# Optimization experiments

Measured on AMD Instinct MI355X. Metric: run time of the kernel, lower is better.

The kernel has to match this reference:

```python
import jax, jax.numpy as jnp
import numpy as np

INPUT_DIM = 1024
HIDDEN_DIM = 2048
NUM_EMB = 4096
EMB_DIM = 256
N = 65536


def setup_inputs() -> dict:
    key = jax.random.key(0)
    ks = jax.random.split(key, 10)
    s = lambda fan_in: 1.0 / np.sqrt(fan_in)
    return {
        "x": jax.random.normal(ks[0], (N, INPUT_DIM), dtype=jnp.float32),
        # encoder: Linear(input_dim, hidden) -> ReLU -> Linear(hidden, emb)
        "W1": jax.random.uniform(ks[1], (INPUT_DIM, HIDDEN_DIM), jnp.float32, -s(INPUT_DIM), s(INPUT_DIM)),
        "b1": jax.random.uniform(ks[2], (HIDDEN_DIM,), jnp.float32, -s(INPUT_DIM), s(INPUT_DIM)),
        "W2": jax.random.uniform(ks[3], (HIDDEN_DIM, EMB_DIM), jnp.float32, -s(HIDDEN_DIM), s(HIDDEN_DIM)),
        "b2": jax.random.uniform(ks[4], (EMB_DIM,), jnp.float32, -s(HIDDEN_DIM), s(HIDDEN_DIM)),
        # codebook (nn.Embedding weight)
        "codebook": jax.random.normal(ks[5], (NUM_EMB, EMB_DIM), dtype=jnp.float32),
        # decoder: Linear(emb, hidden) -> ReLU -> Linear(hidden, input_dim)
        "W3": jax.random.uniform(ks[6], (EMB_DIM, HIDDEN_DIM), jnp.float32, -s(EMB_DIM), s(EMB_DIM)),
        "b3": jax.random.uniform(ks[7], (HIDDEN_DIM,), jnp.float32, -s(EMB_DIM), s(EMB_DIM)),
        "W4": jax.random.uniform(ks[8], (HIDDEN_DIM, INPUT_DIM), jnp.float32, -s(HIDDEN_DIM), s(HIDDEN_DIM)),
        "b4": jax.random.uniform(ks[9], (INPUT_DIM,), jnp.float32, -s(HIDDEN_DIM), s(HIDDEN_DIM)),
    }


def reference(x, W1, b1, W2, b2, codebook, W3, b3, W4, b4):
    # encoder
    h = jax.nn.relu(x @ W1 + b1)
    encoded = h @ W2 + b2                      # [N, E]
    # cdist (squared form; argmin is identical to Euclidean argmin)
    enc_sq = jnp.sum(encoded * encoded, axis=-1, keepdims=True)   # [N, 1]
    cb_sq = jnp.sum(codebook * codebook, axis=-1)                 # [K]
    d2 = enc_sq - 2.0 * (encoded @ codebook.T) + cb_sq            # [N, K]
    indices = jnp.argmin(d2, axis=-1)                             # [N]
    quantized = codebook[indices]                                 # [N, E]
    # decoder
    h2 = jax.nn.relu(quantized @ W3 + b3)
    decoded = h2 @ W4 + b4
    return (quantized, decoded)
```

## Files before the change

### kernel.cpp

```cpp
#include <hip/hip_runtime.h>

#define N_ROWS 65536
#define IN_DIM 1024
#define HID    2048
#define EMB    256
#define NCODE  4096

typedef __attribute__((ext_vector_type(8))) short bf16x8;
typedef __attribute__((ext_vector_type(4))) float f32x4;

__device__ __forceinline__ unsigned short f2bf(float v) {
    unsigned u = __float_as_uint(v);
    u += 0x7FFFu + ((u >> 16) & 1u);
    return (unsigned short)(u >> 16);
}
__device__ __forceinline__ float bf2f(unsigned short h) {
    return __uint_as_float(((unsigned)h) << 16);
}
__device__ __forceinline__ void gload16(const unsigned short* g, unsigned short* l) {
    __builtin_amdgcn_global_load_lds(
        (const __attribute__((address_space(1))) unsigned int*)g,
        (__attribute__((address_space(3))) unsigned int*)l, 16, 0, 0);
}

template<int SPLIT>
__global__ __launch_bounds__(256) void k_conv_w(
    const float* __restrict__ src, unsigned short* __restrict__ dh,
    unsigned short* __restrict__ dl, int NC, int nkt)
{
    const int t = threadIdx.x;
    const int nt = blockIdx.x, kt = blockIdx.y;
    const int kk = t >> 2, j4 = (t & 3) << 2;
    const int k0 = kt << 6, n0 = nt << 4;
    float4 v = *(const float4*)(src + (size_t)(k0 + kk) * NC + n0 + j4);
    size_t tb = ((size_t)nt * nkt + kt) * 1024 + ((kk >> 3) * 128) + (kk & 7);
    float vv[4] = {v.x, v.y, v.z, v.w};
    #pragma unroll
    for (int j = 0; j < 4; ++j) {
        unsigned short h = f2bf(vv[j]);
        dh[tb + (size_t)(j4 + j) * 8] = h;
        if (SPLIT) dl[tb + (size_t)(j4 + j) * 8] = f2bf(vv[j] - bf2f(h));
    }
}

__global__ __launch_bounds__(256) void k_conv_a2(
    const float* __restrict__ src, unsigned short* __restrict__ dh,
    unsigned short* __restrict__ dl, int Kw, int nkt)
{
    const int t = threadIdx.x;
    const int mt = blockIdx.x, kt = blockIdx.y;
    const int rr = t >> 4, k4 = (t & 15) << 2;
    float4 v = *(const float4*)(src + (size_t)(mt * 16 + rr) * Kw + kt * 64 + k4);
    size_t addr = ((size_t)mt * nkt + kt) * 1024 + (k4 >> 3) * 128 + rr * 8 + (k4 & 7);
    ushort4 h = { f2bf(v.x), f2bf(v.y), f2bf(v.z), f2bf(v.w) };
    ushort4 lo = { f2bf(v.x - bf2f(h.x)), f2bf(v.y - bf2f(h.y)),
                   f2bf(v.z - bf2f(h.z)), f2bf(v.w - bf2f(h.w)) };
    *(ushort4*)&dh[addr] = h;
    *(ushort4*)&dl[addr] = lo;
}

__global__ __launch_bounds__(256) void k_conv_cb(
    const float* __restrict__ cb, unsigned short* __restrict__ ch,
    unsigned short* __restrict__ cl_, float* __restrict__ halfsq)
{
    const int t = threadIdx.x;
    const int ct = blockIdx.x;
    const int cl = t >> 4, f = t & 15;
    const int code = (ct << 4) + cl;
    float ssq = 0.f;
    #pragma unroll
    for (int it = 0; it < 4; ++it) {
        const int k4 = (f << 2) + (it << 6);
        float4 v = *(const float4*)(cb + (size_t)code * EMB + k4);
        ssq += v.x * v.x + v.y * v.y + v.z * v.z + v.w * v.w;
        size_t tb = ((size_t)(ct * 4 + (k4 >> 6))) * 1024 + ((k4 >> 3) & 7) * 128 + cl * 8 + (k4 & 7);
        ushort4 h = { f2bf(v.x), f2bf(v.y), f2bf(v.z), f2bf(v.w) };
        *(ushort4*)&ch[tb] = h;
        ushort4 lo = { f2bf(v.x - bf2f(h.x)), f2bf(v.y - bf2f(h.y)),
                       f2bf(v.z - bf2f(h.z)), f2bf(v.w - bf2f(h.w)) };
        *(ushort4*)&cl_[tb] = lo;
    }
    #pragma unroll
    for (int off = 1; off <= 8; off <<= 1) ssq += __shfl_xor(ssq, off);
    if (f == 0) halfsq[code] = 0.5f * ssq;
}

__global__ __launch_bounds__(512, 2) void k_gemm1(
    const unsigned short* __restrict__ At, const unsigned short* __restrict__ Atl,
    int a_nkt,
    const unsigned short* __restrict__ Bh, const unsigned short* __restrict__ Bl,
    int b_nkt, int K,
    const float* __restrict__ bias,
    unsigned short* __restrict__ outt, unsigned short* __restrict__ outt2,
    int out_nkt)
{
    constexpr int BUFSZ = 16384;
    __shared__ __align__(16) unsigned short s_mem[2 * BUFSZ];

    const int t = threadIdx.x;
    const int id = blockIdx.x;
    const int m_low = id & 7, rest = id >> 3;
    const int nb = rest & 15;
    const int m0 = (((rest >> 4) << 3) | m_low) * 128;
    const int nb0 = nb * 128;
    const int lane = t & 63, wv = t >> 6;
    const int wm = wv >> 2, wn = wv & 3;
    const int g = lane >> 4, rr = lane & 15;
    const int nt = K >> 6;

    f32x4 acc[4][2];
    #pragma unroll
    for (int mi = 0; mi < 4; ++mi)
        #pragma unroll
        for (int ni = 0; ni < 2; ++ni) acc[mi][ni] = (f32x4){0.f, 0.f, 0.f, 0.f};

    #define G1_STAGE(buf, ktile)                                                       \
        {                                                                              \
            unsigned short* base_ = &s_mem[(buf) * BUFSZ];                             \
            const size_t ga_ = ((size_t)(m0 / 16 + wv) * a_nkt + (ktile)) * 1024;      \
            const size_t gb_ = ((size_t)((nb0 >> 4) + wv) * b_nkt + (ktile)) * 1024;   \
            _Pragma("unroll")                                                          \
            for (int hf = 0; hf < 2; ++hf) {                                           \
                gload16(At + ga_ + hf * 512 + lane * 8, base_ + wv * 1024 + hf * 512); \
                gload16(Bh + gb_ + hf * 512 + lane * 8, base_ + 8192 + wv * 1024 + hf * 512); \
            }                                                                          \
        }

    #define G1_COMPUTE(buf, ktile)                                                     \
        {                                                                              \
            const unsigned short* base_ = &s_mem[(buf) * BUFSZ];                       \
            __builtin_amdgcn_s_setprio(1);                                             \
            _Pragma("unroll")                                                          \
            for (int s = 0; s < 2; ++s) {                                              \
                const int kb = (s << 2) + g;                                           \
                bf16x8 a_h[4], a_l[4], b_h[2], b_l[2];                                 \
                _Pragma("unroll")                                                      \
                for (int i = 0; i < 4; ++i) {                                          \
                    int aaddr = (wm * 4 + i) * 1024 + kb * 128 + (rr << 3);            \
                    a_h[i] = *(const bf16x8*)&base_[aaddr];                            \
                    a_l[i] = *(const bf16x8*)(Atl +                                    \
                        ((size_t)(m0 / 16 + wm * 4 + i) * a_nkt + (ktile)) * 1024      \
                        + kb * 128 + (rr << 3));                                       \
                }                                                                      \
                _Pragma("unroll")                                                      \
                for (int j = 0; j < 2; ++j) {                                          \
                    int baddr = 8192 + (wn * 2 + j) * 1024 + kb * 128 + (rr << 3);     \
                    b_h[j] = *(const bf16x8*)&base_[baddr];                            \
                    b_l[j] = *(const bf16x8*)(Bl +                                     \
                        ((size_t)((nb0 >> 4) + wn * 2 + j) * b_nkt + (ktile)) * 1024   \
                        + kb * 128 + (rr << 3));                                       \
                }                                                                      \
                _Pragma("unroll")                                                      \
                for (int mi = 0; mi < 4; ++mi)                                         \
                    _Pragma("unroll")                                                  \
                    for (int ni = 0; ni < 2; ++ni) {                                   \
                        acc[mi][ni] = __builtin_amdgcn_mfma_f32_16x16x32_bf16(a_h[mi], b_h[ni], acc[mi][ni], 0, 0, 0); \
                        acc[mi][ni] = __builtin_amdgcn_mfma_f32_16x16x32_bf16(a_l[mi], b_h[ni], acc[mi][ni], 0, 0, 0); \
                        acc[mi][ni] = __builtin_amdgcn_mfma_f32_16x16x32_bf16(a_h[mi], b_l[ni], acc[mi][ni], 0, 0, 0); \
                    }                                                                  \
            }                                                                          \
            __builtin_amdgcn_s_setprio(0);                                             \
        }

    G1_STAGE(0, 0)
    asm volatile("s_waitcnt vmcnt(0)" ::: "memory");
    __builtin_amdgcn_s_barrier();
    __builtin_amdgcn_sched_barrier(0);

    int cur = 0;
    for (int kt = 0; kt < nt; ++kt) {
        if (kt + 1 < nt) G1_STAGE(cur ^ 1, kt + 1)
        G1_COMPUTE(cur, kt)
        asm volatile("s_waitcnt vmcnt(0)" ::: "memory");
        __builtin_amdgcn_s_barrier();
        __builtin_amdgcn_sched_barrier(0);
        cur ^= 1;
    }
    #undef G1_STAGE
    #undef G1_COMPUTE

    for (int pass = 0; pass < 2; ++pass) {
        #pragma unroll
        for (int mi = 0; mi < 4; ++mi)
            #pragma unroll
            for (int ni = 0; ni < 2; ++ni) {
                const int c = wn * 32 + ni * 16 + rr;
                float bb = bias[nb0 + c];
                const int ktl = c >> 6, k = c & 63;
                #pragma unroll
                for (int rg = 0; rg < 4; ++rg) {
                    float v = fmaxf(acc[mi][ni][rg] + bb, 0.f);
                    unsigned short hi = f2bf(v);
                    unsigned short w = (pass == 0) ? hi : f2bf(v - bf2f(hi));
                    int addr = ((wm * 4 + mi) * 2 + ktl) * 1024
                             + ((k >> 3) & 7) * 128 + (g * 4 + rg) * 8 + (k & 7);
                    s_mem[addr] = w;
                }
            }
        __syncthreads();
        unsigned short* dst = (pass == 0) ? outt : outt2;
        #pragma unroll
        for (int it = 0; it < 4; ++it) {
            int f = t + (it << 9);
            int tl = f >> 7, w8 = f & 127;
            size_t gaddr = ((size_t)(m0 / 16 + (tl >> 1)) * out_nkt + (nb0 >> 6) + (tl & 1)) * 1024;
            *(float4*)(dst + gaddr + w8 * 8) = *(const float4*)&s_mem[tl * 1024 + w8 * 8];
        }
        __syncthreads();
    }
}

__global__ __launch_bounds__(512, 1) void k_gemm2(
    const unsigned short* __restrict__ At, const unsigned short* __restrict__ Atl,
    int a_nkt,
    const unsigned short* __restrict__ Bh, const unsigned short* __restrict__ Bl,
    int b_nkt, int K,
    const float* __restrict__ bias, float* __restrict__ out)
{
    constexpr int BUFSZ = 24576;
    __shared__ __align__(16) unsigned short s_mem[2 * BUFSZ];

    const int t = threadIdx.x;
    const int m0 = blockIdx.x * 64;
    const int lane = t & 63, wv = t >> 6;
    const int wm = wv >> 2, wn = wv & 3;
    const int g = lane >> 4, rr = lane & 15;
    const int nt = K >> 6;

    f32x4 acc[2][4];
    #pragma unroll
    for (int mi = 0; mi < 2; ++mi)
        #pragma unroll
        for (int ni = 0; ni < 4; ++ni) acc[mi][ni] = (f32x4){0.f, 0.f, 0.f, 0.f};

    #define G2_STAGE(buf, ktile)                                                       \
        {                                                                              \
            unsigned short* base_ = &s_mem[(buf) * BUFSZ];                             \
            _Pragma("unroll")                                                          \
            for (int jj = 0; jj < 2; ++jj) {                                           \
                const int j_ = wv * 2 + jj;                                            \
                const size_t gb_ = ((size_t)j_ * b_nkt + (ktile)) * 1024;              \
                _Pragma("unroll")                                                      \
                for (int hf = 0; hf < 2; ++hf)                                         \
                    gload16(Bh + gb_ + hf * 512 + lane * 8,                            \
                            base_ + 8192 + j_ * 1024 + hf * 512);                      \
            }                                                                          \
            const int at_ = wv & 3;                                                    \
            const size_t ga_ = ((size_t)(m0 / 16 + at_) * a_nkt + (ktile)) * 1024;     \
            if (wv < 4) {                                                              \
                _Pragma("unroll")                                                      \
                for (int hf = 0; hf < 2; ++hf)                                         \
                    gload16(At + ga_ + hf * 512 + lane * 8,                            \
                            base_ + at_ * 1024 + hf * 512);                            \
            } else {                                                                   \
                _Pragma("unroll")                                                      \
                for (int hf = 0; hf < 2; ++hf)                                         \
                    gload16(Atl + ga_ + hf * 512 + lane * 8,                           \
                            base_ + 4096 + at_ * 1024 + hf * 512);                     \
            }                                                                          \
        }

    #define G2_COMPUTE(buf, ktile)                                                     \
        {                                                                              \
            const unsigned short* base_ = &s_mem[(buf) * BUFSZ];                       \
            __builtin_amdgcn_s_setprio(1);                                             \
            _Pragma("unroll")                                                          \
            for (int s = 0; s < 2; ++s) {                                              \
                const int kb = (s << 2) + g;                                           \
                bf16x8 a_h[2], a_l[2], b_h[4], b_l[4];                                 \
                _Pragma("unroll")                                                      \
                for (int i = 0; i < 2; ++i) {                                          \
                    int aaddr = (wm * 2 + i) * 1024 + kb * 128 + (rr << 3);            \
                    a_h[i] = *(const bf16x8*)&base_[aaddr];                            \
                    a_l[i] = *(const bf16x8*)&base_[4096 + aaddr];                     \
                }                                                                      \
                _Pragma("unroll")                                                      \
                for (int j = 0; j < 4; ++j) {                                          \
                    int baddr = 8192 + (wn * 4 + j) * 1024 + kb * 128 + (rr << 3);     \
                    b_h[j] = *(const bf16x8*)&base_[baddr];                            \
                    b_l[j] = *(const bf16x8*)(Bl +                                     \
                        ((size_t)(wn * 4 + j) * b_nkt + (ktile)) * 1024                \
                        + kb * 128 + (rr << 3));                                       \
                }                                                                      \
                _Pragma("unroll")                                                      \
                for (int mi = 0; mi < 2; ++mi)                                         \
                    _Pragma("unroll")                                                  \
                    for (int ni = 0; ni < 4; ++ni) {                                   \
                        acc[mi][ni] = __builtin_amdgcn_mfma_f32_16x16x32_bf16(a_h[mi], b_h[ni], acc[mi][ni], 0, 0, 0); \
                        acc[mi][ni] = __builtin_amdgcn_mfma_f32_16x16x32_bf16(a_l[mi], b_h[ni], acc[mi][ni], 0, 0, 0); \
                        acc[mi][ni] = __builtin_amdgcn_mfma_f32_16x16x32_bf16(a_h[mi], b_l[ni], acc[mi][ni], 0, 0, 0); \
                    }                                                                  \
            }                                                                          \
            __builtin_amdgcn_s_setprio(0);                                             \
        }

    G2_STAGE(0, 0)
    asm volatile("s_waitcnt vmcnt(0)" ::: "memory");
    __builtin_amdgcn_s_barrier();
    __builtin_amdgcn_sched_barrier(0);

    int cur = 0;
    for (int kt = 0; kt < nt; ++kt) {
        if (kt + 1 < nt) G2_STAGE(cur ^ 1, kt + 1)
        G2_COMPUTE(cur, kt)
        asm volatile("s_waitcnt vmcnt(0)" ::: "memory");
        __builtin_amdgcn_s_barrier();
        __builtin_amdgcn_sched_barrier(0);
        cur ^= 1;
    }
    #undef G2_STAGE
    #undef G2_COMPUTE

    float* sf = (float*)s_mem;
    #pragma unroll
    for (int mi = 0; mi < 2; ++mi)
        #pragma unroll
        for (int ni = 0; ni < 4; ++ni)
            #pragma unroll
            for (int rg = 0; rg < 4; ++rg)
                sf[(wm * 32 + mi * 16 + g * 4 + rg) * 256 + wn * 64 + ni * 16 + rr] = acc[mi][ni][rg];
    __syncthreads();
    #pragma unroll
    for (int it = 0; it < 8; ++it) {
        int f = t + (it << 9);
        int r = f >> 6, c4 = (f & 63) << 2;
        float4 v = *(const float4*)&sf[r * 256 + c4];
        v.x += bias[c4 + 0]; v.y += bias[c4 + 1];
        v.z += bias[c4 + 2]; v.w += bias[c4 + 3];
        *(float4*)(out + (size_t)(m0 + r) * EMB + c4) = v;
    }
}

template<int SPLIT, int AFMT, int OUTT>
__global__ __launch_bounds__(512, 1) void k_layer2(
    const float* __restrict__ A, const unsigned short* __restrict__ At,
    const unsigned short* __restrict__ Atl, int a_nkt,
    int lda, int K,
    const unsigned short* __restrict__ Bh, const unsigned short* __restrict__ Bl,
    int b_nkt, const float* __restrict__ bias, int biasoff,
    float* __restrict__ out, unsigned short* __restrict__ outt,
    unsigned short* __restrict__ outt2,
    int outw, int relu, int init, int ny_log2)
{
    constexpr int BUFSZ = SPLIT ? 32768 : 24576;
    constexpr int AL = 8192;
    constexpr int BH = SPLIT ? 16384 : 8192;
    __shared__ __align__(16) unsigned short s_mem[2 * BUFSZ];

    const int t = threadIdx.x;
    const int id = blockIdx.x;
    const int m_low = id & 7, rest = id >> 3;
    const int nb = rest & ((1 << ny_log2) - 1);
    const int m0 = (((rest >> ny_log2) << 3) | m_low) * 128;
    const int nb0 = nb * 256;
    const int lane = t & 63, wv = t >> 6;
    const int wm = wv >> 2, wn = wv & 3;
    const int g = lane >> 4, rr = lane & 15;
    const int nt = K >> 6;

    f32x4 acc[4][4];
    #pragma unroll
    for (int mi = 0; mi < 4; ++mi)
        #pragma unroll
        for (int ni = 0; ni < 4; ++ni) acc[mi][ni] = (f32x4){0.f, 0.f, 0.f, 0.f};

    #define STAGE_DMA(buf, ktile)                                                      \
        {                                                                              \
            unsigned short* base_ = &s_mem[(buf) * BUFSZ];                             \
            _Pragma("unroll")                                                          \
            for (int jj = 0; jj < 2; ++jj) {                                           \
                const int j_ = wv * 2 + jj;                                            \
                const size_t gt_ = ((size_t)(nb0 / 16 + j_) * b_nkt + (ktile)) * 1024; \
                _Pragma("unroll")                                                      \
                for (int hf = 0; hf < 2; ++hf)                                         \
                    gload16(Bh + gt_ + hf * 512 + lane * 8,                            \
                            base_ + BH + j_ * 1024 + hf * 512);                        \
            }                                                                          \
            if (AFMT >= 1) {                                                           \
                const size_t ga_ = ((size_t)(m0 / 16 + wv) * a_nkt + (ktile)) * 1024;  \
                _Pragma("unroll")                                                      \
                for (int hf = 0; hf < 2; ++hf)                                         \
                    gload16(At + ga_ + hf * 512 + lane * 8,                            \
                            base_ + wv * 1024 + hf * 512);                             \
                if (AFMT == 2) {                                                       \
                    _Pragma("unroll")                                                  \
                    for (int hf = 0; hf < 2; ++hf)                                     \
                        gload16(Atl + ga_ + hf * 512 + lane * 8,                       \
                                base_ + AL + wv * 1024 + hf * 512);                    \
                }                                                                      \
            }                                                                          \
        }

    #define A_LOAD(ktile, pv)                                                          \
        {                                                                              \
            _Pragma("unroll")                                                          \
            for (int it = 0; it < 4; ++it) {                                           \
                int f_ = t + (it << 9);                                                \
                int r_ = f_ >> 4, k4_ = (f_ & 15) << 2;                                \
                pv[it] = *(const float4*)(A + (size_t)(m0 + r_) * lda + (ktile) * 64 + k4_); \
            }                                                                          \
        }

    #define A_WRITE(buf, pv)                                                           \
        {                                                                              \
            unsigned short* base_ = &s_mem[(buf) * BUFSZ];                             \
            _Pragma("unroll")                                                          \
            for (int it = 0; it < 4; ++it) {                                           \
                int f_ = t + (it << 9);                                                \
                int r_ = f_ >> 4, k4_ = (f_ & 15) << 2;                                \
                int mt_ = r_ >> 4, rl_ = r_ & 15, kb_ = k4_ >> 3, e_ = k4_ & 7;        \
                int addr_ = mt_ * 1024 + kb_ * 128 + ((rl_ ^ kb_) << 3) + e_;          \
                float4 v_ = pv[it];                                                    \
                ushort4 hi_, lo_;                                                      \
                hi_.x = f2bf(v_.x); hi_.y = f2bf(v_.y); hi_.z = f2bf(v_.z); hi_.w = f2bf(v_.w); \
                *(ushort4*)&base_[addr_] = hi_;                                        \
                if (SPLIT) {                                                           \
                    lo_.x = f2bf(v_.x - bf2f(hi_.x)); lo_.y = f2bf(v_.y - bf2f(hi_.y)); \
                    lo_.z = f2bf(v_.z - bf2f(hi_.z)); lo_.w = f2bf(v_.w - bf2f(hi_.w)); \
                    *(ushort4*)&base_[AL + addr_] = lo_;                               \
                }                                                                      \
            }                                                                          \
        }

    #define COMPUTE(buf, ktile)                                                        \
        {                                                                              \
            const unsigned short* base_ = &s_mem[(buf) * BUFSZ];                       \
            __builtin_amdgcn_s_setprio(1);                                             \
            _Pragma("unroll")                                                          \
            for (int s = 0; s < 2; ++s) {                                              \
                const int kb = (s << 2) + g;                                           \
                bf16x8 a_h[4], a_l[4], b_h[4], b_l[4];                                 \
                _Pragma("unroll")                                                      \
                for (int i = 0; i < 4; ++i) {                                          \
                    int arow = (AFMT == 0) ? (((rr ^ kb) & 15) << 3) : (rr << 3);      \
                    int aaddr = (wm * 4 + i) * 1024 + kb * 128 + arow;                 \
                    a_h[i] = *(const bf16x8*)&base_[aaddr];                            \
                    if (SPLIT) a_l[i] = *(const bf16x8*)&base_[AL + aaddr];            \
                    int baddr = (wn * 4 + i) * 1024 + kb * 128 + (rr << 3);            \
                    b_h[i] = *(const bf16x8*)&base_[BH + baddr];                       \
                    if (SPLIT)                                                         \
                        b_l[i] = *(const bf16x8*)(Bl +                                 \
                            ((size_t)(nb0 / 16 + wn * 4 + i) * b_nkt + (ktile)) * 1024 \
                            + kb * 128 + (rr << 3));                                   \
                }                                                                      \
                _Pragma("unroll")                                                      \
                for (int mi = 0; mi < 4; ++mi)                                         \
                    _Pragma("unroll")                                                  \
                    for (int ni = 0; ni < 4; ++ni) {                                   \
                        acc[mi][ni] = __builtin_amdgcn_mfma_f32_16x16x32_bf16(a_h[mi], b_h[ni], acc[mi][ni], 0, 0, 0); \
                        if (SPLIT) {                                                   \
                            acc[mi][ni] = __builtin_amdgcn_mfma_f32_16x16x32_bf16(a_l[mi], b_h[ni], acc[mi][ni], 0, 0, 0); \
                            acc[mi][ni] = __builtin_amdgcn_mfma_f32_16x16x32_bf16(a_h[mi], b_l[ni], acc[mi][ni], 0, 0, 0); \
                        }                                                              \
                    }                                                                  \
            }                                                                          \
            __builtin_amdgcn_s_setprio(0);                                             \
        }

    float4 pv[4];
    STAGE_DMA(0, 0)
    if (AFMT == 0) {
        A_LOAD(0, pv)
        A_WRITE(0, pv)
    }
    asm volatile("s_waitcnt vmcnt(0) lgkmcnt(0)" ::: "memory");
    __builtin_amdgcn_s_barrier();
    __builtin_amdgcn_sched_barrier(0);

    int cur = 0;
    for (int kt = 0; kt < nt; ++kt) {
        if (kt + 1 < nt) {
            STAGE_DMA(cur ^ 1, kt + 1)
            if (AFMT == 0) A_LOAD(kt + 1, pv)
        }
        COMPUTE(cur, kt)
        if (AFMT == 0) { if (kt + 1 < nt) A_WRITE(cur ^ 1, pv) }
        asm volatile("s_waitcnt vmcnt(0) lgkmcnt(0)" ::: "memory");
        __builtin_amdgcn_s_barrier();
        __builtin_amdgcn_sched_barrier(0);
        cur ^= 1;
    }
    #undef STAGE_DMA
    #undef A_LOAD
    #undef A_WRITE
    #undef COMPUTE

    if (OUTT == 0) {
        float* sf = (float*)s_mem;
        for (int rm = 0; rm < 2; ++rm) {
            if (wm == rm) {
                #pragma unroll
                for (int mi = 0; mi < 4; ++mi)
                    #pragma unroll
                    for (int ni = 0; ni < 4; ++ni)
                        #pragma unroll
                        for (int rg = 0; rg < 4; ++rg)
                            sf[(mi * 16 + g * 4 + rg) * 256 + wn * 64 + ni * 16 + rr] = acc[mi][ni][rg];
            }
            __syncthreads();
            #pragma unroll
            for (int it = 0; it < 8; ++it) {
                int f = t + (it << 9);
                int r = f >> 6, c4 = (f & 63) << 2;
                float4 v = *(const float4*)&sf[r * 256 + c4];
                int gr = m0 + rm * 64 + r, gc = nb0 + c4;
                float* op = out + (size_t)gr * outw + gc;
                if (init) {
                    v.x += bias[biasoff + gc + 0]; v.y += bias[biasoff + gc + 1];
                    v.z += bias[biasoff + gc + 2]; v.w += bias[biasoff + gc + 3];
                } else {
                    float4 o = *(const float4*)op;
                    v.x += o.x; v.y += o.y; v.z += o.z; v.w += o.w;
                }
                if (relu) {
                    v.x = fmaxf(v.x, 0.f); v.y = fmaxf(v.y, 0.f);
                    v.z = fmaxf(v.z, 0.f); v.w = fmaxf(v.w, 0.f);
                }
                *(float4*)op = v;
            }
            __syncthreads();
        }
    } else {
        const int npass = (OUTT == 2) ? 2 : 1;
        for (int pass = 0; pass < npass; ++pass) {
            #pragma unroll
            for (int mi = 0; mi < 4; ++mi)
                #pragma unroll
                for (int ni = 0; ni < 4; ++ni) {
                    const int c = wn * 64 + ni * 16 + rr;
                    float bb = bias[biasoff + nb0 + c];
                    #pragma unroll
                    for (int rg = 0; rg < 4; ++rg) {
                        float v = acc[mi][ni][rg] + bb;
                        if (relu) v = fmaxf(v, 0.f);
                        unsigned short hi = f2bf(v);
                        unsigned short w = (pass == 0) ? hi : f2bf(v - bf2f(hi));
                        int addr = ((wm * 4 + mi) * 4 + wn) * 1024
                                 + (ni * 2 + (rr >> 3)) * 128 + (g * 4 + rg) * 8 + (rr & 7);
                        s_mem[addr] = w;
                    }
                }
            __syncthreads();
            unsigned short* dst = (pass == 0) ? outt : outt2;
            #pragma unroll
            for (int it = 0; it < 8; ++it) {
                int f = t + (it << 9);
                int tl = f >> 7, w8 = f & 127;
                size_t gaddr = ((size_t)(m0 / 16 + (tl >> 2)) * outw + nb0 / 64 + (tl & 3)) * 1024;
                *(float4*)(dst + gaddr + w8 * 8) = *(const float4*)&s_mem[tl * 1024 + w8 * 8];
            }
            __syncthreads();
        }
    }
}

__global__ __launch_bounds__(512, 1) void k_dist(
    float* encq, const unsigned short* __restrict__ ch,
    const unsigned short* __restrict__ cl,
    const float* __restrict__ hsq, const float* __restrict__ cb,
    unsigned short* __restrict__ qt)
{
    __shared__ __align__(16) unsigned short s_cb[3][16384];
    __shared__ int s_c1[256], s_c2[256];

    const int t = threadIdx.x;
    const int lane = t & 63, wv = t >> 6;
    const int g = lane >> 4, rr = lane & 15;
    const int r0 = blockIdx.x * 256;

    bf16x8 eh[2][8], el[2][8];
    #pragma unroll
    for (int rg = 0; rg < 2; ++rg) {
        const float* ep = encq + (size_t)(r0 + wv * 32 + rg * 16 + rr) * EMB + g * 8;
        #pragma unroll
        for (int s = 0; s < 8; ++s) {
            float4 v0 = *(const float4*)(ep + s * 32);
            float4 v1 = *(const float4*)(ep + s * 32 + 4);
            float vv[8] = {v0.x, v0.y, v0.z, v0.w, v1.x, v1.y, v1.z, v1.w};
            bf16x8 a, b;
            #pragma unroll
            for (int j = 0; j < 8; ++j) {
                unsigned short h = f2bf(vv[j]);
                a[j] = (short)h;
                b[j] = (short)f2bf(vv[j] - bf2f(h));
            }
            eh[rg][s] = a; el[rg][s] = b;
        }
    }
    float b1v[2][4], b2v[2][4]; int i1v[2][4], i2v[2][4];
    #pragma unroll
    for (int rg = 0; rg < 2; ++rg)
        #pragma unroll
        for (int r2 = 0; r2 < 4; ++r2) {
            b1v[rg][r2] = -1e30f; b2v[rg][r2] = -1e30f;
            i1v[rg][r2] = 0; i2v[rg][r2] = 0;
        }

    #define STAGE(buf, c)                                                              \
        {                                                                              \
            const unsigned short* gh_ = ch + (size_t)(c) * 8192 + wv * 1024;           \
            const unsigned short* gl_ = cl + (size_t)(c) * 8192 + wv * 1024;           \
            _Pragma("unroll")                                                          \
            for (int i_ = 0; i_ < 2; ++i_) {                                           \
                gload16(gh_ + i_ * 512 + lane * 8, &s_cb[buf][wv * 1024 + i_ * 512]);  \
                gload16(gl_ + i_ * 512 + lane * 8, &s_cb[buf][8192 + wv * 1024 + i_ * 512]); \
            }                                                                          \
        }

    #define COMPUTE(cur, c, hv_)                                                       \
        {                                                                              \
            f32x4 ahh[2][2], ahl[2][2], alh[2][2];                                     \
            _Pragma("unroll")                                                          \
            for (int rg = 0; rg < 2; ++rg)                                             \
                _Pragma("unroll")                                                      \
                for (int ci = 0; ci < 2; ++ci) {                                       \
                    ahh[rg][ci] = (f32x4){0.f, 0.f, 0.f, 0.f};                         \
                    ahl[rg][ci] = (f32x4){0.f, 0.f, 0.f, 0.f};                         \
                    alh[rg][ci] = (f32x4){0.f, 0.f, 0.f, 0.f};                         \
                }                                                                      \
            __builtin_amdgcn_s_setprio(1);                                             \
            _Pragma("unroll")                                                          \
            for (int s = 0; s < 8; ++s) {                                              \
                const int ktile = s >> 1, kb = ((s & 1) << 2) + g;                     \
                _Pragma("unroll")                                                      \
                for (int ci = 0; ci < 2; ++ci) {                                       \
                    const int off = (ci * 4 + ktile) * 1024 + kb * 128 + rr * 8;       \
                    bf16x8 bh = *(const bf16x8*)&s_cb[cur][off];                       \
                    bf16x8 bl = *(const bf16x8*)&s_cb[cur][8192 + off];                \
                    _Pragma("unroll")                                                  \
                    for (int rg = 0; rg < 2; ++rg) {                                   \
                        ahh[rg][ci] = __builtin_amdgcn_mfma_f32_16x16x32_bf16(eh[rg][s], bh, ahh[rg][ci], 0, 0, 0); \
                        ahl[rg][ci] = __builtin_amdgcn_mfma_f32_16x16x32_bf16(eh[rg][s], bl, ahl[rg][ci], 0, 0, 0); \
                        alh[rg][ci] = __builtin_amdgcn_mfma_f32_16x16x32_bf16(el[rg][s], bh, alh[rg][ci], 0, 0, 0); \
                    }                                                                  \
                }                                                                      \
            }                                                                          \
            __builtin_amdgcn_s_setprio(0);                                             \
            _Pragma("unroll")                                                          \
            for (int rg = 0; rg < 2; ++rg)                                             \
                _Pragma("unroll")                                                      \
                for (int ci = 0; ci < 2; ++ci) {                                       \
                    f32x4 av = ahh[rg][ci] + ahl[rg][ci] + alh[rg][ci];                \
                    const int code = ((c) << 5) + (ci << 4) + rr;                      \
                    const float hs = __shfl(hv_, ci * 16 + rr);                        \
                    _Pragma("unroll")                                                  \
                    for (int r2 = 0; r2 < 4; ++r2) {                                   \
                        float v = av[r2] - hs;                                         \
                        bool bt1 = (v > b1v[rg][r2]) || (v == b1v[rg][r2] && code < i1v[rg][r2]); \
                        bool bt2 = (v > b2v[rg][r2]) || (v == b2v[rg][r2] && code < i2v[rg][r2]); \
                        if (bt1) { b2v[rg][r2] = b1v[rg][r2]; i2v[rg][r2] = i1v[rg][r2]; \
                                   b1v[rg][r2] = v; i1v[rg][r2] = code; }              \
                        else if (bt2) { b2v[rg][r2] = v; i2v[rg][r2] = code; }         \
                    }                                                                  \
                }                                                                      \
        }

    STAGE(0, 0)
    int bufc = 0;
    for (int c = 0; c < 128; ++c) {
        const int bufn = (bufc == 2) ? 0 : bufc + 1;
        if (c + 1 < 128) STAGE(bufn, c + 1)
        float hv_ = hsq[(c << 5) + (lane & 31)];
        if (c + 1 < 128) asm volatile("s_waitcnt vmcnt(5)" ::: "memory");
        else             asm volatile("s_waitcnt vmcnt(0)" ::: "memory");
        __builtin_amdgcn_s_barrier();
        __builtin_amdgcn_sched_barrier(0);
        COMPUTE(bufc, c, hv_)
        bufc = bufn;
    }
    #undef STAGE
    #undef COMPUTE

    #pragma unroll
    for (int off = 1; off <= 8; off <<= 1) {
        #pragma unroll
        for (int rg = 0; rg < 2; ++rg)
            #pragma unroll
            for (int r2 = 0; r2 < 4; ++r2) {
                float ob1 = __shfl_xor(b1v[rg][r2], off), ob2 = __shfl_xor(b2v[rg][r2], off);
                int oi1 = __shfl_xor(i1v[rg][r2], off), oi2 = __shfl_xor(i2v[rg][r2], off);
                bool ofirst = (ob1 > b1v[rg][r2]) || (ob1 == b1v[rg][r2] && oi1 < i1v[rg][r2]);
                if (ofirst) {
                    bool mysec = (b1v[rg][r2] > ob2) || (b1v[rg][r2] == ob2 && i1v[rg][r2] < oi2);
                    b2v[rg][r2] = mysec ? b1v[rg][r2] : ob2; i2v[rg][r2] = mysec ? i1v[rg][r2] : oi2;
                    b1v[rg][r2] = ob1; i1v[rg][r2] = oi1;
                } else {
                    bool osec = (ob1 > b2v[rg][r2]) || (ob1 == b2v[rg][r2] && oi1 < i2v[rg][r2]);
                    b2v[rg][r2] = osec ? ob1 : b2v[rg][r2]; i2v[rg][r2] = osec ? oi1 : i2v[rg][r2];
                }
            }
    }
    if (rr == 0) {
        #pragma unroll
        for (int rg = 0; rg < 2; ++rg)
            #pragma unroll
            for (int r2 = 0; r2 < 4; ++r2) {
                int rl = wv * 32 + rg * 16 + g * 4 + r2;
                s_c1[rl] = i1v[rg][r2]; s_c2[rl] = i2v[rg][r2];
            }
    }
    __syncthreads();

    for (int rloc = 0; rloc < 32; ++rloc) {
        const int row = wv * 32 + rloc;
        const int c1 = s_c1[row], c2 = s_c2[row];
        float4 ev = *(const float4*)(encq + (size_t)(r0 + row) * EMB + lane * 4);
        float4 v1 = *(const float4*)(cb + (size_t)c1 * EMB + lane * 4);
        float4 v2 = *(const float4*)(cb + (size_t)c2 * EMB + lane * 4);
        float d1 = ev.x * v1.x + ev.y * v1.y + ev.z * v1.z + ev.w * v1.w;
        float d2 = ev.x * v2.x + ev.y * v2.y + ev.z * v2.z + ev.w * v2.w;
        #pragma unroll
        for (int off = 1; off <= 32; off <<= 1) {
            d1 += __shfl_xor(d1, off);
            d2 += __shfl_xor(d2, off);
        }
        if (lane == 0) {
            float s1 = d1 - hsq[c1], s2 = d2 - hsq[c2];
            bool keep1 = (s1 > s2) || (s1 == s2 && c1 < c2);
            s_c1[row] = keep1 ? c1 : c2;
        }
    }
    __syncthreads();
    #pragma unroll
    for (int it = 0; it < 32; ++it) {
        int f = t + (it << 9);
        int row = f >> 6, c4 = (f & 63) << 2;
        int bi = s_c1[row];
        float4 qv = *(const float4*)(cb + (size_t)bi * EMB + c4);
        const int R = r0 + row;
        *(float4*)(encq + (size_t)R * EMB + c4) = qv;
        const int k4 = c4 & 63;
        size_t qaddr = ((size_t)(R >> 4) * 4 + (c4 >> 6)) * 1024
                     + (k4 >> 3) * 128 + (R & 15) * 8 + (k4 & 7);
        ushort4 qh = { f2bf(qv.x), f2bf(qv.y), f2bf(qv.z), f2bf(qv.w) };
        *(ushort4*)&qt[qaddr] = qh;
    }
}

__global__ __launch_bounds__(256) void k_dec_fb(
    const float* __restrict__ qz,
    const float* __restrict__ W3, const float* __restrict__ b3,
    const float* __restrict__ W4, const float* __restrict__ b4,
    float* __restrict__ outd) {
    __shared__ float s_q[8][EMB];
    __shared__ float s_h2[8][HID];
    const int t = threadIdx.x;
    const int row0 = blockIdx.x * 8;
    #pragma unroll
    for (int r = 0; r < 8; ++r) s_q[r][t] = qz[(size_t)(row0 + r) * EMB + t];
    __syncthreads();
    for (int gg = 0; gg < 8; ++gg) {
        const int j = (gg << 8) + t;
        float acc[8];
        #pragma unroll
        for (int r = 0; r < 8; ++r) acc[r] = 0.f;
        const float* wp = W3 + j;
        for (int e = 0; e < EMB; e += 4) {
            const float w0 = wp[(size_t)(e + 0) * HID];
            const float w1v = wp[(size_t)(e + 1) * HID];
            const float w2v = wp[(size_t)(e + 2) * HID];
            const float w3v = wp[(size_t)(e + 3) * HID];
            #pragma unroll
            for (int r = 0; r < 8; ++r) {
                const float4 qv = *reinterpret_cast<const float4*>(&s_q[r][e]);
                acc[r] = fmaf(qv.x, w0, acc[r]);
                acc[r] = fmaf(qv.y, w1v, acc[r]);
                acc[r] = fmaf(qv.z, w2v, acc[r]);
                acc[r] = fmaf(qv.w, w3v, acc[r]);
            }
        }
        const float bb = b3[j];
        #pragma unroll
        for (int r = 0; r < 8; ++r) s_h2[r][j] = fmaxf(acc[r] + bb, 0.f);
    }
    __syncthreads();
    float acc4[8][4];
    #pragma unroll
    for (int r = 0; r < 8; ++r)
        #pragma unroll
        for (int ci = 0; ci < 4; ++ci) acc4[r][ci] = 0.f;
    const float* w4p = W4 + t;
    for (int k = 0; k < HID; k += 4) {
        float wv[4][4];
        #pragma unroll
        for (int ki = 0; ki < 4; ++ki)
            #pragma unroll
            for (int ci = 0; ci < 4; ++ci)
                wv[ki][ci] = w4p[(size_t)(k + ki) * IN_DIM + (ci << 8)];
        #pragma unroll
        for (int r = 0; r < 8; ++r) {
            const float4 hv = *reinterpret_cast<const float4*>(&s_h2[r][k]);
            #pragma unroll
            for (int ci = 0; ci < 4; ++ci) {
                acc4[r][ci] = fmaf(hv.x, wv[0][ci], acc4[r][ci]);
                acc4[r][ci] = fmaf(hv.y, wv[1][ci], acc4[r][ci]);
                acc4[r][ci] = fmaf(hv.z, wv[2][ci], acc4[r][ci]);
                acc4[r][ci] = fmaf(hv.w, wv[3][ci], acc4[r][ci]);
            }
        }
    }
    #pragma unroll
    for (int ci = 0; ci < 4; ++ci) {
        const float bb = b4[(ci << 8) + t];
        #pragma unroll
        for (int r = 0; r < 8; ++r)
            outd[(size_t)(row0 + r) * IN_DIM + (ci << 8) + t] = acc4[r][ci] + bb;
    }
}

extern "C" void kernel_launch(void* const* d_in, const int* in_sizes, int n_in,
                              void* d_out, int out_size, void* d_ws, size_t ws_size,
                              hipStream_t stream) {
    const float* x  = (const float*)d_in[0];
    const float* W1 = (const float*)d_in[1];
    const float* b1 = (const float*)d_in[2];
    const float* W2 = (const float*)d_in[3];
    const float* b2 = (const float*)d_in[4];
    const float* cb = (const float*)d_in[5];
    const float* W3 = (const float*)d_in[6];
    const float* b3 = (const float*)d_in[7];
    const float* W4 = (const float*)d_in[8];
    const float* b4 = (const float*)d_in[9];

    float* outq = (float*)d_out;
    float* outd = outq + (size_t)N_ROWS * EMB;

    unsigned short* ou = (unsigned short*)outd;
    unsigned short* W1Th = ou;
    unsigned short* W1Tl = ou + 2097152;
    unsigned short* W2Th = ou + 4194304;
    unsigned short* W2Tl = ou + 4718592;
    unsigned short* cbh  = ou + 5242880;
    unsigned short* cbl  = ou + 6291456;
    float* halfsq = outd + 3670016;
    unsigned short* h_hi = (unsigned short*)(outd + 4194304);
    unsigned short* h_lo = h_hi + 33554432;
    unsigned short* qt = (unsigned short*)(outd + 58720256);
    float* enc = outq;

    const bool fastdec = ws_size >= (size_t)72351744;
    unsigned short* W3Th = (unsigned short*)d_ws;
    unsigned short* W4Th = W3Th + 524288;
    unsigned short* h2t  = (unsigned short*)((char*)d_ws + 5242880);
    unsigned short* xt_hi = h2t;
    unsigned short* xt_lo = h2t + 16777216;

    k_conv_w<1><<<dim3(128, 16), 256, 0, stream>>>(W1, W1Th, W1Tl, HID, 16);
    k_conv_w<1><<<dim3(16, 32), 256, 0, stream>>>(W2, W2Th, W2Tl, EMB, 32);
    k_conv_cb<<<256, 256, 0, stream>>>(cb, cbh, cbl, halfsq);
    if (fastdec) {
        k_conv_w<0><<<dim3(128, 4), 256, 0, stream>>>(W3, W3Th, nullptr, HID, 4);
        k_conv_w<0><<<dim3(64, 32), 256, 0, stream>>>(W4, W4Th, nullptr, IN_DIM, 32);
    }
    if (fastdec) {
        for (int s = 0; s < 4; ++s) {
            k_conv_a2<<<dim3(1024, 16), 256, 0, stream>>>(
                x + (size_t)s * 16777216, xt_hi, xt_lo, IN_DIM, 16);
            k_gemm1<<<2048, 512, 0, stream>>>(
                xt_hi, xt_lo, 16, W1Th, W1Tl, 16, IN_DIM, b1, h_hi, h_lo, 32);
            k_gemm2<<<256, 512, 0, stream>>>(
                h_hi, h_lo, 32, W2Th, W2Tl, 32, HID, b2,
                enc + (size_t)s * 4194304);
        }
    } else {
        for (int q = 0; q < 4; ++q) {
            k_layer2<1, 0, 2><<<1024, 512, 0, stream>>>(
                x, nullptr, nullptr, 0, IN_DIM, IN_DIM,
                W1Th + (size_t)q * 524288, W1Tl + (size_t)q * 524288, 16,
                b1, q * 512, nullptr, h_hi, h_lo, 8, 1, 0, 1);
            k_layer2<1, 2, 0><<<512, 512, 0, stream>>>(
                nullptr, h_hi, h_lo, 8, 0, 512,
                W2Th + (size_t)q * 8192, W2Tl + (size_t)q * 8192, 32,
                b2, 0, enc, nullptr, nullptr, EMB, 0, q == 0, 0);
        }
    }
    k_dist<<<256, 512, 0, stream>>>(enc, cbh, cbl, halfsq, cb, qt);
    if (fastdec) {
        for (int s = 0; s < 4; ++s) {
            const size_t roff = (size_t)s * 16384;
            k_layer2<0, 1, 1><<<1024, 512, 0, stream>>>(
                nullptr, qt + (size_t)s * 4194304, nullptr, 4, 0, EMB,
                W3Th, nullptr, 4,
                b3, 0, nullptr, h2t, nullptr, 32, 1, 0, 3);
            k_layer2<0, 1, 0><<<512, 512, 0, stream>>>(
                nullptr, h2t, nullptr, 32, 0, HID,
                W4Th, nullptr, 32,
                b4, 0, outd + roff * IN_DIM, nullptr, nullptr, IN_DIM, 0, 1, 2);
        }
    } else {
        k_dec_fb<<<N_ROWS / 8, 256, 0, stream>>>(outq, W3, b3, W4, b4, outd);
    }
}
```

Baseline: 2.199 ms.

## Triple-buffer LDS staging with partial vmcnt waits in bf16 GEMM kernels

Switches k_gemm2 and the non-split, pre-transposed k_layer2 variant from double to triple-buffered LDS tiles. The next tile's DMA is issued before computing the current one, and the wait uses vmcnt(6), so only the older tile's loads must land. This lets one tile load stay in flight during compute. It is meant to cut the load-latency stall at each barrier, at the cost of 50% more LDS per block (up to 144KB) and an extra barrier before the epilogue.

```diff
diff --git a/kernel.cpp b/kernel.cpp
--- a/kernel.cpp
+++ b/kernel.cpp
@@ -218,7 +218,7 @@
     const float* __restrict__ bias, float* __restrict__ out)
 {
     constexpr int BUFSZ = 24576;
-    __shared__ __align__(16) unsigned short s_mem[2 * BUFSZ];
+    __shared__ __align__(16) unsigned short s_mem[3 * BUFSZ];
 
     const int t = threadIdx.x;
     const int m0 = blockIdx.x * 64;
@@ -295,21 +295,23 @@
         }
 
     G2_STAGE(0, 0)
-    asm volatile("s_waitcnt vmcnt(0)" ::: "memory");
-    __builtin_amdgcn_s_barrier();
-    __builtin_amdgcn_sched_barrier(0);
-
-    int cur = 0;
+    int bufc = 0;
     for (int kt = 0; kt < nt; ++kt) {
-        if (kt + 1 < nt) G2_STAGE(cur ^ 1, kt + 1)
-        G2_COMPUTE(cur, kt)
-        asm volatile("s_waitcnt vmcnt(0)" ::: "memory");
+        const int bufn = (bufc == 2) ? 0 : bufc + 1;
+        if (kt + 1 < nt) {
+            G2_STAGE(bufn, kt + 1)
+            asm volatile("s_waitcnt vmcnt(6)" ::: "memory");
+        } else {
+            asm volatile("s_waitcnt vmcnt(0)" ::: "memory");
+        }
         __builtin_amdgcn_s_barrier();
         __builtin_amdgcn_sched_barrier(0);
-        cur ^= 1;
+        G2_COMPUTE(bufc, kt)
+        bufc = bufn;
     }
     #undef G2_STAGE
     #undef G2_COMPUTE
+    __builtin_amdgcn_s_barrier();
 
     float* sf = (float*)s_mem;
     #pragma unroll
@@ -343,9 +345,10 @@
     int outw, int relu, int init, int ny_log2)
 {
     constexpr int BUFSZ = SPLIT ? 32768 : 24576;
+    constexpr int NBUF  = SPLIT ? 2 : 3;
     constexpr int AL = 8192;
     constexpr int BH = SPLIT ? 16384 : 8192;
-    __shared__ __align__(16) unsigned short s_mem[2 * BUFSZ];
+    __shared__ __align__(16) unsigned short s_mem[NBUF * BUFSZ];
 
     const int t = threadIdx.x;
     const int id = blockIdx.x;
@@ -457,28 +460,46 @@
             __builtin_amdgcn_s_setprio(0);                                             \
         }
 
-    float4 pv[4];
-    STAGE_DMA(0, 0)
-    if (AFMT == 0) {
-        A_LOAD(0, pv)
-        A_WRITE(0, pv)
-    }
-    asm volatile("s_waitcnt vmcnt(0) lgkmcnt(0)" ::: "memory");
-    __builtin_amdgcn_s_barrier();
-    __builtin_amdgcn_sched_barrier(0);
-
-    int cur = 0;
-    for (int kt = 0; kt < nt; ++kt) {
-        if (kt + 1 < nt) {
-            STAGE_DMA(cur ^ 1, kt + 1)
-            if (AFMT == 0) A_LOAD(kt + 1, pv)
-        }
-        COMPUTE(cur, kt)
-        if (AFMT == 0) { if (kt + 1 < nt) A_WRITE(cur ^ 1, pv) }
+    if (SPLIT || AFMT == 0) {
+        float4 pv[4];
+        STAGE_DMA(0, 0)
+        if (AFMT == 0) {
+            A_LOAD(0, pv)
+            A_WRITE(0, pv)
+        }
         asm volatile("s_waitcnt vmcnt(0) lgkmcnt(0)" ::: "memory");
         __builtin_amdgcn_s_barrier();
         __builtin_amdgcn_sched_barrier(0);
-        cur ^= 1;
+        int cur = 0;
+        for (int kt = 0; kt < nt; ++kt) {
+            if (kt + 1 < nt) {
+                STAGE_DMA(cur ^ 1, kt + 1)
+                if (AFMT == 0) A_LOAD(kt + 1, pv)
+            }
+            COMPUTE(cur, kt)
+            if (AFMT == 0) { if (kt + 1 < nt) A_WRITE(cur ^ 1, pv) }
+            asm volatile("s_waitcnt vmcnt(0) lgkmcnt(0)" ::: "memory");
+            __builtin_amdgcn_s_barrier();
+            __builtin_amdgcn_sched_barrier(0);
+            cur ^= 1;
+        }
+    } else {
+        STAGE_DMA(0, 0)
+        int bufc = 0;
+        for (int kt = 0; kt < nt; ++kt) {
+            const int bufn = (bufc == 2) ? 0 : bufc + 1;
+            if (kt + 1 < nt) {
+                STAGE_DMA(bufn, kt + 1)
+                asm volatile("s_waitcnt vmcnt(6)" ::: "memory");
+            } else {
+                asm volatile("s_waitcnt vmcnt(0)" ::: "memory");
+            }
+            __builtin_amdgcn_s_barrier();
+            __builtin_amdgcn_sched_barrier(0);
+            COMPUTE(bufc, kt)
+            bufc = bufn;
+        }
+        __builtin_amdgcn_s_barrier();
     }
     #undef STAGE_DMA
     #undef A_LOAD
```

Measured after the change: 2.153 ms, median of 2. -2.1%, faster.
